# Optimization experiments

Measured on AMD Instinct MI355X. Metric: run time of the kernel, lower is better.

The kernel has to match this reference:

```python
import jax, jax.numpy as jnp
import numpy as np

A, B, D, H = 64, 256, 128, 512  # seq rows, columns (encoder batch / decode loop), n_dims, hidden


def _lstm_step(Wih, Whh, bih, bhh, h, c, x):
    # x: [N, D], h/c: [N, H]; PyTorch gate order i, f, g, o
    gates = x @ Wih.T + bih + h @ Whh.T + bhh  # [N, 4H]
    i, f, g, o = jnp.split(gates, 4, axis=-1)
    c = jax.nn.sigmoid(f) * c + jax.nn.sigmoid(i) * jnp.tanh(g)
    h = jax.nn.sigmoid(o) * jnp.tanh(c)
    return h, c


def setup_inputs() -> dict:
    key = jax.random.key(0)
    ks = jax.random.split(key, 12)
    s = 0.05
    inp = {
        "input_tensor": jax.random.normal(ks[0], (A, B, D), jnp.float32),
        "enc_Wih": jax.random.normal(ks[1], (4 * H, D), jnp.float32) * s,
        "enc_Whh": jax.random.normal(ks[2], (4 * H, H), jnp.float32) * s,
        "enc_bih": jax.random.normal(ks[3], (4 * H,), jnp.float32) * s,
        "enc_bhh": jax.random.normal(ks[4], (4 * H,), jnp.float32) * s,
        "dec_Wih": jax.random.normal(ks[5], (4 * H, D), jnp.float32) * s,
        "dec_Whh": jax.random.normal(ks[6], (4 * H, H), jnp.float32) * s,
        "dec_bih": jax.random.normal(ks[7], (4 * H,), jnp.float32) * s,
        "dec_bhh": jax.random.normal(ks[8], (4 * H,), jnp.float32) * s,
        "lin_W": jax.random.normal(ks[9], (D, H), jnp.float32) * s,
        "lin_b": jax.random.normal(ks[10], (D,), jnp.float32) * s,
    }
    return inp


def reference(input_tensor, enc_Wih, enc_Whh, enc_bih, enc_bhh,
              dec_Wih, dec_Whh, dec_bih, dec_bhh, lin_W, lin_b):
    a, b, d = input_tensor.shape
    h_dim = enc_Whh.shape[1]
    dt = input_tensor.dtype

    # ---- encoder: seq-first LSTM over dim0 (len a), batch = b ----
    def e_step(hc, x_t):
        h, c = hc
        h, c = _lstm_step(enc_Wih, enc_Whh, enc_bih, enc_bhh, h, c, x_t)
        return (h, c), None

    h0 = jnp.zeros((b, h_dim), dt)
    (hN, cN), _ = jax.lax.scan(e_step, (h0, h0), input_tensor)
    # hidden[0][:, -1].unsqueeze(1): keep only the LAST batch element -> [1, H]
    dh, dc = hN[-1:], cN[-1:]

    # ---- decoder: loop i = b-1 .. 0; emit linear(h) then run length-a LSTM on column i ----
    def col_step(hc, x_col):  # x_col: [a, d]
        h, c = hc
        out_i = (h @ lin_W.T + lin_b)[0]  # [d], emitted BEFORE processing the column

        def t_step(hc2, x_t):
            h2, c2 = hc2
            h2, c2 = _lstm_step(dec_Wih, dec_Whh, dec_bih, dec_bhh, h2, c2, x_t[None])
            return (h2, c2), None

        (h, c), _ = jax.lax.scan(t_step, (h, c), x_col)
        return (h, c), out_i

    x_cols = jnp.flip(jnp.transpose(input_tensor, (1, 0, 2)), 0)  # [b, a, d], reversed i
    _, outs = jax.lax.scan(col_step, (dh, dc), x_cols)  # [b, d] in reversed order
    outs = jnp.flip(outs, 0)
    # outputs[:, i, :] = [1, d] row broadcast across all a rows
    return jnp.broadcast_to(outs[None, :, :], (a, b, d))
```

## Files before the change

### kernel.cpp

```cpp
#include <hip/hip_runtime.h>
#include <math.h>

#define A_ 64
#define B_ 256
#define D_ 128
#define H_ 512
#define STOT 16384
#define NWG 32

#define XCC_GETREG_IMM (20 | (31 << 11))

#define OFF_XT    0
#define N_XT      (A_*D_*B_)
#define OFF_HT0   (OFF_XT + N_XT)
#define OFF_HT1   (OFF_HT0 + H_*B_)
#define OFF_CT    (OFF_HT1 + H_*B_)
#define OFF_HTAP  (OFF_CT + H_*B_)
#define OFF_HB64  (OFF_HTAP + B_*H_)
#define OFF_CINIT (OFF_HB64 + 4*H_)
#define OFF_ELECT (OFF_CINIT + H_)

__device__ __forceinline__ float sigf(float x) {
  return __builtin_amdgcn_rcpf(1.0f + __expf(-x));
}
__device__ __forceinline__ float tanhfast(float x) {
  return 1.0f - 2.0f * __builtin_amdgcn_rcpf(__expf(2.0f * x) + 1.0f);
}

__device__ __forceinline__ unsigned long long load_nt(const unsigned long long* p) {
  unsigned long long v;
  asm volatile("global_load_dwordx2 %0, %1, off nt\n\ts_waitcnt vmcnt(0)"
               : "=&v"(v) : "v"(p) : "memory");
  return v;
}
__device__ __forceinline__ unsigned long long load_inv(const unsigned long long* p) {
  unsigned long long v;
  asm volatile("buffer_inv sc0\n\t"
               "global_load_dwordx2 %0, %1, off nt\n\ts_waitcnt vmcnt(0)"
               : "=&v"(v) : "v"(p) : "memory");
  return v;
}
__device__ __forceinline__ void store_nt(unsigned long long* p, unsigned long long v) {
  asm volatile("global_store_dwordx2 %0, %1, off nt" :: "v"(p), "v"(v) : "memory");
}

__global__ void init1(const float* __restrict__ in0, float* __restrict__ ws) {
  float* XT  = ws + OFF_XT;
  float* HT0 = ws + OFF_HT0;
  float* CT  = ws + OFF_CT;
  int stride = gridDim.x * blockDim.x;
  for (int idx = blockIdx.x * blockDim.x + threadIdx.x; idx < N_XT; idx += stride) {
    int t = idx >> 15;
    int k = (idx >> 8) & 127;
    int b = idx & 255;
    XT[idx] = in0[t * (B_ * D_) + b * D_ + k];
    if (idx < H_ * B_) { HT0[idx] = 0.f; CT[idx] = 0.f; }
  }
}

__global__ __launch_bounds__(256) void enc_step(
    const float* __restrict__ XT, const float* __restrict__ Wih,
    const float* __restrict__ Whh, const float* __restrict__ bih,
    const float* __restrict__ bhh, const float* __restrict__ Hin,
    float* __restrict__ Hout, float* __restrict__ C, int t) {
  __shared__ float Wt[16 * 68];
  __shared__ float XHt[16 * 32];
  __shared__ float gs[64 * 33];
  const int tid = threadIdx.x;
  const int jt = blockIdx.x;
  const int bt = blockIdx.y;
  const int rr = tid >> 4;
  const int bb = tid & 15;

  float acc[4][2];
#pragma unroll
  for (int i = 0; i < 4; ++i) {
    int r = 4 * rr + i;
    int Row = ((r >> 4) << 9) + (jt << 4) + (r & 15);
    float bv = bih[Row] + bhh[Row];
    acc[i][0] = bv; acc[i][1] = bv;
  }

  for (int kt = 0; kt < 40; ++kt) {
    int k0 = kt << 4;
    __syncthreads();
#pragma unroll
    for (int e = 0; e < 4; ++e) {
      int idx = tid + (e << 8);
      int kk = idx & 15, r = idx >> 4;
      int Row = ((r >> 4) << 9) + (jt << 4) + (r & 15);
      int k = k0 + kk;
      float v = (k < D_) ? Wih[Row * D_ + k] : Whh[Row * H_ + (k - D_)];
      Wt[kk * 68 + r] = v;
    }
#pragma unroll
    for (int e = 0; e < 2; ++e) {
      int idx = tid + (e << 8);
      int kk = idx >> 5, b = idx & 31;
      int k = k0 + kk;
      int gb = (bt << 5) + b;
      float v = (k < D_) ? XT[(t * D_ + k) * B_ + gb] : Hin[(k - D_) * B_ + gb];
      XHt[kk * 32 + b] = v;
    }
    __syncthreads();
#pragma unroll
    for (int kk = 0; kk < 16; ++kk) {
      const float4 wv = *(const float4*)&Wt[kk * 68 + 4 * rr];
      const float2 xv = *(const float2*)&XHt[kk * 32 + 2 * bb];
      acc[0][0] += wv.x * xv.x; acc[0][1] += wv.x * xv.y;
      acc[1][0] += wv.y * xv.x; acc[1][1] += wv.y * xv.y;
      acc[2][0] += wv.z * xv.x; acc[2][1] += wv.z * xv.y;
      acc[3][0] += wv.w * xv.x; acc[3][1] += wv.w * xv.y;
    }
  }
  __syncthreads();
#pragma unroll
  for (int i = 0; i < 4; ++i) {
    gs[(4 * rr + i) * 33 + 2 * bb]     = acc[i][0];
    gs[(4 * rr + i) * 33 + 2 * bb + 1] = acc[i][1];
  }
  __syncthreads();
#pragma unroll
  for (int e = 0; e < 2; ++e) {
    int idx = tid + (e << 8);
    int jj = idx >> 5, b = idx & 31;
    int gb = (bt << 5) + b;
    float iv = gs[jj * 33 + b];
    float fv = gs[(16 + jj) * 33 + b];
    float gv = gs[(32 + jj) * 33 + b];
    float ov = gs[(48 + jj) * 33 + b];
    int addr = ((jt << 4) + jj) * B_ + gb;
    float c = C[addr];
    c = sigf(fv) * c + sigf(iv) * tanhf(gv);
    C[addr] = c;
    Hout[addr] = sigf(ov) * tanhf(c);
  }
}

__global__ void init2(float* __restrict__ ws) {
  const float* Hfin = ws + OFF_HT0;
  const float* CT   = ws + OFF_CT;
  unsigned long long* HB = (unsigned long long*)(ws + OFF_HB64);
  float* CIN  = ws + OFF_CINIT;
  float* HTAP = ws + OFF_HTAP;
  int* EL     = (int*)(ws + OFF_ELECT);
  int j = threadIdx.x;
  float hj = Hfin[j * B_ + 255];
  HB[H_ + j] = (unsigned long long)__float_as_uint(hj);
  HB[j]      = 0xFFFFFFFF00000000ull;
  CIN[j]  = CT[j * B_ + 255];
  HTAP[j] = hj;
  if (j < 8) EL[j] = 0;
  if (j == 8) EL[8] = -1;
}

__global__ __launch_bounds__(1024) void decoder(
    const float* __restrict__ in0, const float* __restrict__ Wih,
    const float* __restrict__ Whh, const float* __restrict__ bih,
    const float* __restrict__ bhh, float* __restrict__ ws) {
  unsigned long long* HB = (unsigned long long*)(ws + OFF_HB64);
  float* HTAP = ws + OFF_HTAP;
  const float* CIN = ws + OFF_CINIT;

  __shared__ float part[2][16 * 64];
  __shared__ float hstage[H_];
  __shared__ int role;

  const int tid = threadIdx.x;

  if (tid == 0) {
    unsigned xcc = ((unsigned)__builtin_amdgcn_s_getreg(XCC_GETREG_IMM)) & 7u;
    int* EL = (int*)(ws + OFF_ELECT);
    int r = __hip_atomic_fetch_add(&EL[xcc], 1, __ATOMIC_RELAXED,
                                   __HIP_MEMORY_SCOPE_AGENT);
    int myrole = -1;
    if (r < NWG) {
      if (r == NWG - 1) {
        int exp = -1;
        __hip_atomic_compare_exchange_strong(&EL[8], &exp, (int)xcc,
            __ATOMIC_RELAXED, __ATOMIC_RELAXED, __HIP_MEMORY_SCOPE_AGENT);
      }
      int wx;
      do {
        wx = __hip_atomic_load(&EL[8], __ATOMIC_RELAXED, __HIP_MEMORY_SCOPE_AGENT);
        if (wx == -1) __builtin_amdgcn_s_sleep(2);
      } while (wx == -1);
      if (wx == (int)xcc) myrole = r;
    }
    role = myrole;
  }
  __syncthreads();
  if (role < 0) return;
  const int w = role;

  const int v = tid >> 6;
  const int l = tid & 63;
  const int R = ((l >> 4) << 9) + (w << 4) + (l & 15);

  float4 wa[8];
#pragma unroll
  for (int k = 0; k < 8; ++k)
    wa[k] = *(const float4*)&Whh[R * H_ + (v << 5) + 4 * k];
  float4 wx0 = *(const float4*)&Wih[R * D_ + (v << 3)];
  float4 wx1 = *(const float4*)&Wih[R * D_ + (v << 3) + 4];

  float bias = 0.f, c = 0.f;
  if (v == 0) {
    bias = bih[R] + bhh[R];
    if (l < 16) c = CIN[(w << 4) + l];
  }

  const int pe = (v << 5) + (l & 31);

  for (int s = 0; s < STOT; ++s) {
    const int tt = s & 63;
    const int bc = 255 - (s >> 6);
    const float* xp = in0 + (tt * B_ + bc) * D_ + (v << 3);
    float4 x0 = *(const float4*)xp;
    float4 x1 = *(const float4*)(xp + 4);

    unsigned long long* slot = &HB[(((s + 1) & 1) << 9) + pe];
    unsigned long long pk;
    int spins = 0;
    for (;;) {
      pk = ((++spins & 63) == 0) ? load_inv(slot) : load_nt(slot);
      if (__all((unsigned)(pk >> 32) == (unsigned)s)) break;
    }
    if (l < 32) hstage[pe] = __uint_as_float((unsigned)pk);

    float p = wx0.x * x0.x + wx0.y * x0.y + wx0.z * x0.z + wx0.w * x0.w
            + wx1.x * x1.x + wx1.y * x1.y + wx1.z * x1.z + wx1.w * x1.w;

    const float4* hp = (const float4*)&hstage[v << 5];
#pragma unroll
    for (int k = 0; k < 8; ++k) {
      float4 h4 = hp[k];
      p += wa[k].x * h4.x + wa[k].y * h4.y + wa[k].z * h4.z + wa[k].w * h4.w;
    }
    part[s & 1][(v << 6) + l] = p;
    __syncthreads();

    if (v == 0) {
      float g = bias;
#pragma unroll
      for (int j = 0; j < 16; ++j) g += part[s & 1][(j << 6) + l];
      const int e = l & 15;
      float vi = __shfl(g, e);
      float vf = __shfl(g, e + 16);
      float vg = __shfl(g, e + 32);
      float vo = __shfl(g, e + 48);
      if (l < 16) {
        c = sigf(vf) * c + sigf(vi) * tanhfast(vg);
        float hn = sigf(vo) * tanhfast(c);
        if ((s & 63) == 63) {
          int q = (s >> 6) + 1;
          if (q < 256) HTAP[q * H_ + (w << 4) + l] = hn;
        }
        unsigned long long opk =
            ((unsigned long long)(unsigned)(s + 1) << 32) | __float_as_uint(hn);
        store_nt(&HB[((s & 1) << 9) + (w << 4) + l], opk);
      }
    }
  }
}

__global__ __launch_bounds__(128) void out_proj(
    const float* __restrict__ ws, const float* __restrict__ linW,
    const float* __restrict__ linb, float* __restrict__ out) {
  const float* HTAP = ws + OFF_HTAP;
  __shared__ float hs[H_];
  const int b = blockIdx.x;
  const int i = 255 - b;
  const int d = threadIdx.x;
  *(float4*)&hs[4 * d] = *(const float4*)&HTAP[i * H_ + 4 * d];
  __syncthreads();
  float acc = linb[d];
#pragma unroll 8
  for (int k = 0; k < H_; k += 4) {
    float4 w4 = *(const float4*)&linW[d * H_ + k];
    acc += w4.x * hs[k] + w4.y * hs[k + 1] + w4.z * hs[k + 2] + w4.w * hs[k + 3];
  }
  for (int a = 0; a < A_; ++a)
    out[(a * B_ + b) * D_ + d] = acc;
}

extern "C" void kernel_launch(void* const* d_in, const int* in_sizes, int n_in,
                              void* d_out, int out_size, void* d_ws, size_t ws_size,
                              hipStream_t stream) {
  const float* in0  = (const float*)d_in[0];
  const float* eWih = (const float*)d_in[1];
  const float* eWhh = (const float*)d_in[2];
  const float* ebih = (const float*)d_in[3];
  const float* ebhh = (const float*)d_in[4];
  const float* dWih = (const float*)d_in[5];
  const float* dWhh = (const float*)d_in[6];
  const float* dbih = (const float*)d_in[7];
  const float* dbhh = (const float*)d_in[8];
  const float* linW = (const float*)d_in[9];
  const float* linb = (const float*)d_in[10];
  float* ws = (float*)d_ws;
  float* out = (float*)d_out;

  init1<<<2048, 256, 0, stream>>>(in0, ws);

  const float* XT = ws + OFF_XT;
  for (int t = 0; t < 64; ++t) {
    float* Hin  = ws + ((t & 1) ? OFF_HT1 : OFF_HT0);
    float* Hout = ws + ((t & 1) ? OFF_HT0 : OFF_HT1);
    enc_step<<<dim3(32, 8), 256, 0, stream>>>(XT, eWih, eWhh, ebih, ebhh,
                                              Hin, Hout, ws + OFF_CT, t);
  }
  init2<<<1, 512, 0, stream>>>(ws);
  decoder<<<256, 1024, 0, stream>>>(in0, dWih, dWhh, dbih, dbhh, ws);
  out_proj<<<256, 128, 0, stream>>>(ws, linW, linb, out);
}
```

Before: 22.49 ms.

## Run encoder only on last batch column inside fused persistent decoder kernel

Only the last batch element of the encoder's final state is used, and LSTM batch columns are independent. So the full 256-column encoder, its input transpose and its 64 per-step launches are replaced by 64 extra single-column recurrent steps in the persistent decoder kernel, using the encoder weights. Gate activations are also unified into one exp/rcp form selected per lane, so sigmoid and tanh share one code path. This removes about 65 kernel launches and the batched encoder GEMMs. In exchange it adds 64 serial cross-workgroup handoff steps and reloads the weights between phases.

```diff
diff --git a/kernel.cpp b/kernel.cpp
--- a/kernel.cpp
+++ b/kernel.cpp
@@ -5,7 +5,8 @@
 #define B_ 256
 #define D_ 128
 #define H_ 512
-#define STOT 16384
+#define STEPS_ENC 64
+#define STEPS_TOT (64 + 16384)
 #define NWG 32
 
 #define XCC_GETREG_IMM (20 | (31 << 11))
@@ -20,9 +21,6 @@
 #define OFF_CINIT (OFF_HB64 + 4*H_)
 #define OFF_ELECT (OFF_CINIT + H_)
 
-__device__ __forceinline__ float sigf(float x) {
-  return __builtin_amdgcn_rcpf(1.0f + __expf(-x));
-}
 __device__ __forceinline__ float tanhfast(float x) {
   return 1.0f - 2.0f * __builtin_amdgcn_rcpf(__expf(2.0f * x) + 1.0f);
 }
@@ -44,123 +42,113 @@
   asm volatile("global_store_dwordx2 %0, %1, off nt" :: "v"(p), "v"(v) : "memory");
 }
 
-__global__ void init1(const float* __restrict__ in0, float* __restrict__ ws) {
-  float* XT  = ws + OFF_XT;
-  float* HT0 = ws + OFF_HT0;
-  float* CT  = ws + OFF_CT;
-  int stride = gridDim.x * blockDim.x;
-  for (int idx = blockIdx.x * blockDim.x + threadIdx.x; idx < N_XT; idx += stride) {
-    int t = idx >> 15;
-    int k = (idx >> 8) & 127;
-    int b = idx & 255;
-    XT[idx] = in0[t * (B_ * D_) + b * D_ + k];
-    if (idx < H_ * B_) { HT0[idx] = 0.f; CT[idx] = 0.f; }
-  }
-}
-
-__global__ __launch_bounds__(256) void enc_step(
-    const float* __restrict__ XT, const float* __restrict__ Wih,
-    const float* __restrict__ Whh, const float* __restrict__ bih,
-    const float* __restrict__ bhh, const float* __restrict__ Hin,
-    float* __restrict__ Hout, float* __restrict__ C, int t) {
-  __shared__ float Wt[16 * 68];
-  __shared__ float XHt[16 * 32];
-  __shared__ float gs[64 * 33];
-  const int tid = threadIdx.x;
-  const int jt = blockIdx.x;
-  const int bt = blockIdx.y;
-  const int rr = tid >> 4;
-  const int bb = tid & 15;
-
-  float acc[4][2];
-#pragma unroll
-  for (int i = 0; i < 4; ++i) {
-    int r = 4 * rr + i;
-    int Row = ((r >> 4) << 9) + (jt << 4) + (r & 15);
-    float bv = bih[Row] + bhh[Row];
-    acc[i][0] = bv; acc[i][1] = bv;
-  }
-
-  for (int kt = 0; kt < 40; ++kt) {
-    int k0 = kt << 4;
-    __syncthreads();
-#pragma unroll
-    for (int e = 0; e < 4; ++e) {
-      int idx = tid + (e << 8);
-      int kk = idx & 15, r = idx >> 4;
-      int Row = ((r >> 4) << 9) + (jt << 4) + (r & 15);
-      int k = k0 + kk;
-      float v = (k < D_) ? Wih[Row * D_ + k] : Whh[Row * H_ + (k - D_)];
-      Wt[kk * 68 + r] = v;
-    }
-#pragma unroll
-    for (int e = 0; e < 2; ++e) {
-      int idx = tid + (e << 8);
-      int kk = idx >> 5, b = idx & 31;
-      int k = k0 + kk;
-      int gb = (bt << 5) + b;
-      float v = (k < D_) ? XT[(t * D_ + k) * B_ + gb] : Hin[(k - D_) * B_ + gb];
-      XHt[kk * 32 + b] = v;
-    }
-    __syncthreads();
-#pragma unroll
-    for (int kk = 0; kk < 16; ++kk) {
-      const float4 wv = *(const float4*)&Wt[kk * 68 + 4 * rr];
-      const float2 xv = *(const float2*)&XHt[kk * 32 + 2 * bb];
-      acc[0][0] += wv.x * xv.x; acc[0][1] += wv.x * xv.y;
-      acc[1][0] += wv.y * xv.x; acc[1][1] += wv.y * xv.y;
-      acc[2][0] += wv.z * xv.x; acc[2][1] += wv.z * xv.y;
-      acc[3][0] += wv.w * xv.x; acc[3][1] += wv.w * xv.y;
-    }
-  }
-  __syncthreads();
-#pragma unroll
-  for (int i = 0; i < 4; ++i) {
-    gs[(4 * rr + i) * 33 + 2 * bb]     = acc[i][0];
-    gs[(4 * rr + i) * 33 + 2 * bb + 1] = acc[i][1];
-  }
-  __syncthreads();
-#pragma unroll
-  for (int e = 0; e < 2; ++e) {
-    int idx = tid + (e << 8);
-    int jj = idx >> 5, b = idx & 31;
-    int gb = (bt << 5) + b;
-    float iv = gs[jj * 33 + b];
-    float fv = gs[(16 + jj) * 33 + b];
-    float gv = gs[(32 + jj) * 33 + b];
-    float ov = gs[(48 + jj) * 33 + b];
-    int addr = ((jt << 4) + jj) * B_ + gb;
-    float c = C[addr];
-    c = sigf(fv) * c + sigf(iv) * tanhf(gv);
-    C[addr] = c;
-    Hout[addr] = sigf(ov) * tanhf(c);
-  }
-}
-
-__global__ void init2(float* __restrict__ ws) {
-  const float* Hfin = ws + OFF_HT0;
-  const float* CT   = ws + OFF_CT;
+__global__ void init0(float* __restrict__ ws) {
   unsigned long long* HB = (unsigned long long*)(ws + OFF_HB64);
-  float* CIN  = ws + OFF_CINIT;
-  float* HTAP = ws + OFF_HTAP;
-  int* EL     = (int*)(ws + OFF_ELECT);
+  int* EL = (int*)(ws + OFF_ELECT);
   int j = threadIdx.x;
-  float hj = Hfin[j * B_ + 255];
-  HB[H_ + j] = (unsigned long long)__float_as_uint(hj);
+  HB[H_ + j] = 0ull;
   HB[j]      = 0xFFFFFFFF00000000ull;
-  CIN[j]  = CT[j * B_ + 255];
-  HTAP[j] = hj;
   if (j < 8) EL[j] = 0;
   if (j == 8) EL[8] = -1;
 }
 
-__global__ __launch_bounds__(1024) void decoder(
-    const float* __restrict__ in0, const float* __restrict__ Wih,
-    const float* __restrict__ Whh, const float* __restrict__ bih,
-    const float* __restrict__ bhh, float* __restrict__ ws) {
+template<int PHASE>
+__device__ __forceinline__ void lstm_phase(
+    const float* __restrict__ in0,
+    const float* __restrict__ Wih, const float* __restrict__ Whh,
+    const float* __restrict__ bih, const float* __restrict__ bhh,
+    unsigned long long* __restrict__ HB, float* __restrict__ HTAP,
+    float (*part)[16 * 64], float* hstage,
+    int w, int v, int l, float& c,
+    float actA, float actB, float actC)
+{
+  const int R = ((l >> 4) << 9) + (w << 4) + (l & 15);
+
+  float4 wa[8];
+#pragma unroll
+  for (int k = 0; k < 8; ++k)
+    wa[k] = *(const float4*)&Whh[R * H_ + (v << 5) + 4 * k];
+  float4 wx0 = *(const float4*)&Wih[R * D_ + (v << 3)];
+  float4 wx1 = *(const float4*)&Wih[R * D_ + (v << 3) + 4];
+
+  float bias = 0.f;
+  if (v == 0) bias = bih[R] + bhh[R];
+
+  const int pe = (v << 5) + (l & 31);
+
+  const int s0 = (PHASE == 0) ? 0 : STEPS_ENC;
+  const int s1 = (PHASE == 0) ? STEPS_ENC : STEPS_TOT;
+
+  for (int s = s0; s < s1; ++s) {
+    const float* xp;
+    if (PHASE == 0) {
+      xp = in0 + (s * B_ + 255) * D_ + (v << 3);
+    } else {
+      const int sd = s - STEPS_ENC;
+      const int tt = sd & 63;
+      const int bc = 255 - (sd >> 6);
+      xp = in0 + (tt * B_ + bc) * D_ + (v << 3);
+    }
+    float4 x0 = *(const float4*)xp;
+    float4 x1 = *(const float4*)(xp + 4);
+
+    unsigned long long* slot = &HB[(((s + 1) & 1) << 9) + pe];
+    unsigned long long pk;
+    int spins = 0;
+    for (;;) {
+      pk = ((++spins & 63) == 0) ? load_inv(slot) : load_nt(slot);
+      if (__all((unsigned)(pk >> 32) == (unsigned)s)) break;
+    }
+    if (l < 32) hstage[pe] = __uint_as_float((unsigned)pk);
+
+    float p = wx0.x * x0.x + wx0.y * x0.y + wx0.z * x0.z + wx0.w * x0.w
+            + wx1.x * x1.x + wx1.y * x1.y + wx1.z * x1.z + wx1.w * x1.w;
+
+    const float4* hp = (const float4*)&hstage[v << 5];
+#pragma unroll
+    for (int k = 0; k < 8; ++k) {
+      float4 h4 = hp[k];
+      p += wa[k].x * h4.x + wa[k].y * h4.y + wa[k].z * h4.z + wa[k].w * h4.w;
+    }
+    part[s & 1][(v << 6) + l] = p;
+    __syncthreads();
+
+    if (v == 0) {
+      float g = bias;
+#pragma unroll
+      for (int j = 0; j < 16; ++j) g += part[s & 1][(j << 6) + l];
+      float a = fmaf(actA,
+                     __builtin_amdgcn_rcpf(__expf(actB * g) + 1.0f), actC);
+      const int e = l & 15;
+      float ai = __shfl(a, e);
+      float af = __shfl(a, e + 16);
+      float ag = __shfl(a, e + 32);
+      float ao = __shfl(a, e + 48);
+      if (l < 16) {
+        c = af * c + ai * ag;
+        float hn = ao * tanhfast(c);
+        if ((s & 63) == 63) {
+          int q = s >> 6;
+          if (q < 256) HTAP[q * H_ + (w << 4) + l] = hn;
+        }
+        unsigned long long opk =
+            ((unsigned long long)(unsigned)(s + 1) << 32) | __float_as_uint(hn);
+        store_nt(&HB[((s & 1) << 9) + (w << 4) + l], opk);
+      }
+    }
+  }
+}
+
+__global__ __launch_bounds__(1024) void fused(
+    const float* __restrict__ in0,
+    const float* __restrict__ eWih, const float* __restrict__ eWhh,
+    const float* __restrict__ ebih, const float* __restrict__ ebhh,
+    const float* __restrict__ dWih, const float* __restrict__ dWhh,
+    const float* __restrict__ dbih, const float* __restrict__ dbhh,
+    float* __restrict__ ws)
+{
   unsigned long long* HB = (unsigned long long*)(ws + OFF_HB64);
   float* HTAP = ws + OFF_HTAP;
-  const float* CIN = ws + OFF_CINIT;
 
   __shared__ float part[2][16 * 64];
   __shared__ float hstage[H_];
@@ -195,73 +183,18 @@
 
   const int v = tid >> 6;
   const int l = tid & 63;
-  const int R = ((l >> 4) << 9) + (w << 4) + (l & 15);
-
-  float4 wa[8];
-#pragma unroll
-  for (int k = 0; k < 8; ++k)
-    wa[k] = *(const float4*)&Whh[R * H_ + (v << 5) + 4 * k];
-  float4 wx0 = *(const float4*)&Wih[R * D_ + (v << 3)];
-  float4 wx1 = *(const float4*)&Wih[R * D_ + (v << 3) + 4];
-
-  float bias = 0.f, c = 0.f;
-  if (v == 0) {
-    bias = bih[R] + bhh[R];
-    if (l < 16) c = CIN[(w << 4) + l];
-  }
-
-  const int pe = (v << 5) + (l & 31);
-
-  for (int s = 0; s < STOT; ++s) {
-    const int tt = s & 63;
-    const int bc = 255 - (s >> 6);
-    const float* xp = in0 + (tt * B_ + bc) * D_ + (v << 3);
-    float4 x0 = *(const float4*)xp;
-    float4 x1 = *(const float4*)(xp + 4);
-
-    unsigned long long* slot = &HB[(((s + 1) & 1) << 9) + pe];
-    unsigned long long pk;
-    int spins = 0;
-    for (;;) {
-      pk = ((++spins & 63) == 0) ? load_inv(slot) : load_nt(slot);
-      if (__all((unsigned)(pk >> 32) == (unsigned)s)) break;
-    }
-    if (l < 32) hstage[pe] = __uint_as_float((unsigned)pk);
-
-    float p = wx0.x * x0.x + wx0.y * x0.y + wx0.z * x0.z + wx0.w * x0.w
-            + wx1.x * x1.x + wx1.y * x1.y + wx1.z * x1.z + wx1.w * x1.w;
-
-    const float4* hp = (const float4*)&hstage[v << 5];
-#pragma unroll
-    for (int k = 0; k < 8; ++k) {
-      float4 h4 = hp[k];
-      p += wa[k].x * h4.x + wa[k].y * h4.y + wa[k].z * h4.z + wa[k].w * h4.w;
-    }
-    part[s & 1][(v << 6) + l] = p;
-    __syncthreads();
-
-    if (v == 0) {
-      float g = bias;
-#pragma unroll
-      for (int j = 0; j < 16; ++j) g += part[s & 1][(j << 6) + l];
-      const int e = l & 15;
-      float vi = __shfl(g, e);
-      float vf = __shfl(g, e + 16);
-      float vg = __shfl(g, e + 32);
-      float vo = __shfl(g, e + 48);
-      if (l < 16) {
-        c = sigf(vf) * c + sigf(vi) * tanhfast(vg);
-        float hn = sigf(vo) * tanhfast(c);
-        if ((s & 63) == 63) {
-          int q = (s >> 6) + 1;
-          if (q < 256) HTAP[q * H_ + (w << 4) + l] = hn;
-        }
-        unsigned long long opk =
-            ((unsigned long long)(unsigned)(s + 1) << 32) | __float_as_uint(hn);
-        store_nt(&HB[((s & 1) << 9) + (w << 4) + l], opk);
-      }
-    }
-  }
+
+  const int gate = l >> 4;
+  const float actA = (gate == 2) ? -2.0f :  1.0f;
+  const float actB = (gate == 2) ?  2.0f : -1.0f;
+  const float actC = (gate == 2) ?  1.0f :  0.0f;
+
+  float c = 0.f;
+
+  lstm_phase<0>(in0, eWih, eWhh, ebih, ebhh, HB, HTAP, part, hstage,
+                w, v, l, c, actA, actB, actC);
+  lstm_phase<1>(in0, dWih, dWhh, dbih, dbhh, HB, HTAP, part, hstage,
+                w, v, l, c, actA, actB, actC);
 }
 
 __global__ __launch_bounds__(128) void out_proj(
@@ -301,16 +234,8 @@
   float* ws = (float*)d_ws;
   float* out = (float*)d_out;
 
-  init1<<<2048, 256, 0, stream>>>(in0, ws);
-
-  const float* XT = ws + OFF_XT;
-  for (int t = 0; t < 64; ++t) {
-    float* Hin  = ws + ((t & 1) ? OFF_HT1 : OFF_HT0);
-    float* Hout = ws + ((t & 1) ? OFF_HT0 : OFF_HT1);
-    enc_step<<<dim3(32, 8), 256, 0, stream>>>(XT, eWih, eWhh, ebih, ebhh,
-                                              Hin, Hout, ws + OFF_CT, t);
-  }
-  init2<<<1, 512, 0, stream>>>(ws);
-  decoder<<<256, 1024, 0, stream>>>(in0, dWih, dWhh, dbih, dbhh, ws);
+  init0<<<1, 512, 0, stream>>>(ws);
+  fused<<<256, 1024, 0, stream>>>(in0, eWih, eWhh, ebih, ebhh,
+                                  dWih, dWhh, dbih, dbhh, ws);
   out_proj<<<256, 128, 0, stream>>>(ws, linW, linb, out);
 }
```

Result: faster. 19.81 ms (-11.9%).
